# Kernel optimization log

Measured on AMD Instinct MI355X. Metric: run time of the kernel, lower is better.

## Reference

```python
import jax, jax.numpy as jnp
import numpy as np

EPS = 1e-6

def setup_inputs() -> dict:
    key = jax.random.key(0)
    k1, k2, k3 = jax.random.split(key, 3)
    B, N, D = 1, 2048, 1024
    x = jax.random.normal(k1, (B, N, D), dtype=jnp.float32)
    W_qvk = jax.random.normal(k2, (D, 3 * D), dtype=jnp.float32) * (D ** -0.5)
    b_qvk = jax.random.normal(k3, (3 * D,), dtype=jnp.float32) * 0.02
    return {"x": x, "W_qvk": W_qvk, "b_qvk": b_qvk, "head_num": 16}


def _forward(x, W_qvk, b_qvk, head_num):
    B, N, D = x.shape
    qvk = x @ W_qvk + b_qvk                       # (B, N, 3D)
    # torch.chunk order in source: q, v, k
    def to_heads(t):
        return t.reshape(B, N, head_num, D // head_num).transpose(0, 2, 1, 3)  # (B,h,N,e)
    q, v, k = (to_heads(t) for t in jnp.split(qvk, 3, axis=-1))
    e = q.shape[-1]
    # causal linear attention, bucket_size=1
    q = jax.nn.softmax(q, axis=-1) * (e ** -0.5)  # (B,h,N,e)
    k = jnp.exp(k)
    k_cumsum = jnp.cumsum(k, axis=2)              # (B,h,N,e)
    # per-position outer product k_i (x) v_i, then causal prefix-sum over N
    kv = jnp.einsum('bhnd,bhne->bhnde', k, v)     # (B,h,N,e,e)
    kv_cumsum = jnp.cumsum(kv, axis=2)            # (B,h,N,e,e)
    denom = jnp.einsum('bhnd,bhnd->bhn', q, k_cumsum + EPS)   # (B,h,N)
    out = jnp.einsum('bhnd,bhnde->bhne', q, kv_cumsum) / denom[..., None]
    # concat heads: (B,h,N,e) -> (B,N,D)
    return out.transpose(0, 2, 1, 3).reshape(B, N, D)


def reference(x, W_qvk, b_qvk, head_num):
    return _forward(x, W_qvk, b_qvk, head_num)
```

## Files before the change

kernel.cpp:

```cpp
#include <hip/hip_runtime.h>
#include <stdint.h>

#define NTOK 2048
#define NCH 32

typedef __attribute__((ext_vector_type(8))) short bf16x8;
typedef __attribute__((ext_vector_type(8))) unsigned short ushort8v;
typedef __attribute__((ext_vector_type(4))) float f32x4;

__device__ __forceinline__ unsigned short f2bf(float f) {
  unsigned u = __float_as_uint(f);
  u += 0x7fffu + ((u >> 16) & 1u);
  return (unsigned short)(u >> 16);
}
__device__ __forceinline__ float bf2f(unsigned short s) {
  return __uint_as_float(((unsigned)s) << 16);
}

__global__ __launch_bounds__(256) void k_prep_inputs(const float* __restrict__ x,
                                                     unsigned short* __restrict__ xb,
                                                     const float* __restrict__ W,
                                                     unsigned short* __restrict__ Wt) {
  int bid = blockIdx.x;
  if (bid < 2048) {
    int i = (bid * 256 + threadIdx.x) * 4;
    float4 v = *(const float4*)(x + i);
    ushort4 o = { f2bf(v.x), f2bf(v.y), f2bf(v.z), f2bf(v.w) };
    *(ushort4*)(xb + i) = o;
  } else {
    __shared__ float tile[32][33];
    int id = bid - 2048;
    int bx = id % 96, by = id / 96;
    int tx = threadIdx.x & 31, ty = threadIdx.x >> 5;
    int c0 = bx * 32;
    int r0 = by * 32;
#pragma unroll
    for (int j = 0; j < 32; j += 8)
      tile[ty + j][tx] = W[(size_t)(r0 + ty + j) * 3072 + c0 + tx];
    __syncthreads();
#pragma unroll
    for (int j = 0; j < 32; j += 8)
      Wt[(size_t)(c0 + ty + j) * 1024 + r0 + tx] = f2bf(tile[tx][ty + j]);
  }
}

__global__ __launch_bounds__(768, 1) void k_gemm_fused(const unsigned short* __restrict__ xb,
                                                       const unsigned short* __restrict__ wt,
                                                       const float* __restrict__ bias,
                                                       unsigned short* __restrict__ qh,
                                                       unsigned short* __restrict__ kh,
                                                       unsigned short* __restrict__ kt,
                                                       unsigned short* __restrict__ vt) {
  __shared__ __align__(16) unsigned short As[2][128][64];
  __shared__ __align__(16) unsigned short Bs[2][192][64];
  const int t = threadIdx.x;
  const int lane = t & 63;
  const int wave = t >> 6;
  const int wr = wave / 3;
  const int wc = wave % 3;
  const int rowBase = blockIdx.y * 128;
  const int colBase = blockIdx.x * 192;
  const int fr = lane & 15;
  const int khalf = lane >> 4;

  const bool isA = t < 256;
  const int nL = isA ? 4 : 3;
  const int bstr = isA ? 16384 : 24576;
  const unsigned short* gsrc[4];
  char* ldst[4];
#pragma unroll
  for (int j = 0; j < 4; ++j) {
    int idx = isA ? (t + j * 256) : (t - 256 + j * 512);
    if (j >= nL) idx = 0;
    int row = idx >> 3;
    int ssl = (idx & 7) ^ (row & 7);
    gsrc[j] = (isA ? xb + (size_t)(rowBase + row) * 1024
                   : wt + (size_t)(colBase + row) * 1024) + ssl * 8;
    ldst[j] = (isA ? (char*)As : (char*)Bs) + idx * 16;
  }

#define STG(buf, kt0) do {                                                                \
    _Pragma("unroll")                                                                     \
    for (int j_ = 0; j_ < 4; ++j_)                                                        \
      if (j_ < nL)                                                                        \
        __builtin_amdgcn_global_load_lds(                                                 \
            (const __attribute__((address_space(1))) void*)(gsrc[j_] + (kt0) * 64),       \
            (__attribute__((address_space(3))) void*)(ldst[j_] + (buf) * bstr), 16, 0, 0);\
  } while (0)

#define VMW_STEADY() do {                                                                 \
    if (isA) asm volatile("s_waitcnt vmcnt(4)" ::: "memory");                             \
    else     asm volatile("s_waitcnt vmcnt(3)" ::: "memory");                             \
  } while (0)
#define VMCNT0() asm volatile("s_waitcnt vmcnt(0)" ::: "memory")
#define LGKM0()  asm volatile("s_waitcnt lgkmcnt(0)" ::: "memory")
#define BAR()    __builtin_amdgcn_s_barrier()

  f32x4 acc[2][4] = {};
  const int fs0 = khalf ^ (fr & 7);

#define LOAD_FRAGS(cur, af, bff) do {                                                     \
    _Pragma("unroll")                                                                     \
    for (int m = 0; m < 2; ++m) {                                                         \
      const unsigned short* r = &As[cur][wr * 32 + m * 16 + fr][0];                       \
      af[m][0] = *(const bf16x8*)(r + fs0 * 8);                                           \
      af[m][1] = *(const bf16x8*)(r + (fs0 ^ 4) * 8);                                     \
    }                                                                                     \
    _Pragma("unroll")                                                                     \
    for (int n = 0; n < 4; ++n) {                                                         \
      const unsigned short* r = &Bs[cur][wc * 64 + n * 16 + fr][0];                       \
      bff[n][0] = *(const bf16x8*)(r + fs0 * 8);                                          \
      bff[n][1] = *(const bf16x8*)(r + (fs0 ^ 4) * 8);                                    \
    }                                                                                     \
  } while (0)

#define DO_MFMA(af, bff) do {                                                             \
    _Pragma("unroll")                                                                     \
    for (int m = 0; m < 2; ++m)                                                           \
      _Pragma("unroll")                                                                   \
      for (int n = 0; n < 4; ++n) {                                                       \
        acc[m][n] = __builtin_amdgcn_mfma_f32_16x16x32_bf16(af[m][0], bff[n][0], acc[m][n], 0, 0, 0); \
        acc[m][n] = __builtin_amdgcn_mfma_f32_16x16x32_bf16(af[m][1], bff[n][1], acc[m][n], 0, 0, 0); \
      }                                                                                   \
  } while (0)

  STG(0, 0);
  STG(1, 1);
#pragma unroll 1
  for (int ktile = 0; ktile < 14; ++ktile) {
    const int cur = ktile & 1;
    VMW_STEADY();
    BAR();
    bf16x8 af[2][2], bff[4][2];
    LOAD_FRAGS(cur, af, bff);
    LGKM0();
    __builtin_amdgcn_sched_barrier(0);
    BAR();
    STG(cur, ktile + 2);
    __builtin_amdgcn_s_setprio(1);
    DO_MFMA(af, bff);
    __builtin_amdgcn_s_setprio(0);
  }
  {
    VMW_STEADY();
    BAR();
    bf16x8 af[2][2], bff[4][2];
    LOAD_FRAGS(0, af, bff);
    DO_MFMA(af, bff);
  }
  {
    VMCNT0();
    BAR();
    bf16x8 af[2][2], bff[4][2];
    LOAD_FRAGS(1, af, bff);
    DO_MFMA(af, bff);
  }
#undef STG
#undef LOAD_FRAGS
#undef DO_MFMA

  const int g2 = khalf;
  const int ocol = lane & 15;
  const int col0 = colBase + wc * 64;
  const int region = col0 >> 10;
  const int h = (col0 & 1023) >> 6;
  const int r0 = rowBase + wr * 32;
  const int cch = r0 >> 6;
  const int lbase = (wr & 1) * 32;
  float bv[4];
#pragma unroll
  for (int n = 0; n < 4; ++n) bv[n] = bias[col0 + 16 * n + ocol];

  if (region == 0) {
#pragma unroll
    for (int m = 0; m < 2; ++m) {
#pragma unroll
      for (int i = 0; i < 4; ++i) {
        float v[4];
#pragma unroll
        for (int n = 0; n < 4; ++n) v[n] = acc[m][n][i] + bv[n];
        float mx = fmaxf(fmaxf(v[0], v[1]), fmaxf(v[2], v[3]));
#pragma unroll
        for (int off = 1; off <= 8; off <<= 1) mx = fmaxf(mx, __shfl_xor(mx, off));
        float s = 0.f;
#pragma unroll
        for (int n = 0; n < 4; ++n) { v[n] = __expf(v[n] - mx); s += v[n]; }
#pragma unroll
        for (int off = 1; off <= 8; off <<= 1) s += __shfl_xor(s, off);
        float inv = 0.125f / s;
        int tok = r0 + 16 * m + 4 * g2 + i;
        unsigned short* qrow = qh + ((size_t)h * NTOK + tok) * 64;
#pragma unroll
        for (int n = 0; n < 4; ++n) qrow[16 * n + ocol] = f2bf(v[n] * inv);
      }
    }
  } else if (region == 1) {
    unsigned short* vb = vt + (size_t)(h * NCH + cch) * 4096;
#pragma unroll
    for (int m = 0; m < 2; ++m) {
      int tl = lbase + 16 * m + 4 * g2;
#pragma unroll
      for (int n = 0; n < 4; ++n) {
        int e = 16 * n + ocol;
        ushort4 p = { f2bf(acc[m][n][0] + bv[n]), f2bf(acc[m][n][1] + bv[n]),
                      f2bf(acc[m][n][2] + bv[n]), f2bf(acc[m][n][3] + bv[n]) };
        *(ushort4*)&vb[(size_t)e * 64 + tl] = p;
      }
    }
  } else {
    unsigned short* kb = kt + (size_t)(h * NCH + cch) * 4096;
#pragma unroll
    for (int m = 0; m < 2; ++m) {
      int tl = lbase + 16 * m + 4 * g2;
#pragma unroll
      for (int n = 0; n < 4; ++n) {
        int e = 16 * n + ocol;
        float kv[4];
#pragma unroll
        for (int i = 0; i < 4; ++i) kv[i] = __expf(acc[m][n][i] + bv[n]);
        ushort4 p = { f2bf(kv[0]), f2bf(kv[1]), f2bf(kv[2]), f2bf(kv[3]) };
        *(ushort4*)&kb[(size_t)e * 64 + tl] = p;
#pragma unroll
        for (int i = 0; i < 4; ++i)
          kh[((size_t)h * NTOK + r0 + 16 * m + 4 * g2 + i) * 64 + e] = p[i];
      }
    }
  }
}

__global__ __launch_bounds__(256) void k_chunk_sums(const unsigned short* __restrict__ kt,
                                                    const unsigned short* __restrict__ vt,
                                                    float* __restrict__ Sc,
                                                    float* __restrict__ zc) {
  int h = blockIdx.x >> 5, c = blockIdx.x & 31;
  __shared__ __align__(16) unsigned short Kt[64][72], Vt[64][72];
  int t = threadIdx.x, lane = t & 63, w = t >> 6;
  int fr = lane & 15, g = lane >> 4, fko = g * 8;
  const unsigned short* kg = kt + (size_t)(h * NCH + c) * 4096;
  const unsigned short* vg = vt + (size_t)(h * NCH + c) * 4096;
  for (int s = t; s < 512; s += 256) {
    int r = s >> 3, c8 = (s & 7) * 8;
    *(ushort8v*)&Kt[r][c8] = *(const ushort8v*)&kg[r * 64 + c8];
    *(ushort8v*)&Vt[r][c8] = *(const ushort8v*)&vg[r * 64 + c8];
  }
  __syncthreads();
  bf16x8 ka[2];
#pragma unroll
  for (int ks = 0; ks < 2; ++ks) ka[ks] = *(const bf16x8*)&Kt[16 * w + fr][32 * ks + fko];
  f32x4 s4[4] = {};
#pragma unroll
  for (int nb = 0; nb < 4; ++nb)
#pragma unroll
    for (int ks = 0; ks < 2; ++ks) {
      bf16x8 vf = *(const bf16x8*)&Vt[16 * nb + fr][32 * ks + fko];
      s4[nb] = __builtin_amdgcn_mfma_f32_16x16x32_bf16(ka[ks], vf, s4[nb], 0, 0, 0);
    }
  float* so = Sc + (size_t)(h * NCH + c) * 4096;
#pragma unroll
  for (int nb = 0; nb < 4; ++nb) {
    float4 o = { s4[nb][0], s4[nb][1], s4[nb][2], s4[nb][3] };
    *(float4*)&so[(size_t)(16 * nb + fr) * 64 + 16 * w + 4 * g] = o;
  }
  if (w == 0) {
    float z = 0.f;
#pragma unroll
    for (int j = 0; j < 8; ++j) {
      bf16x8 kv = *(const bf16x8*)&Kt[lane][j * 8];
#pragma unroll
      for (int e = 0; e < 8; ++e) z += bf2f((unsigned short)kv[e]);
    }
    zc[(size_t)(h * NCH + c) * 64 + lane] = z;
  }
}

__global__ __launch_bounds__(256) void k_scan(const float* __restrict__ Sc,
                                              unsigned short* __restrict__ Sp,
                                              const float* __restrict__ zc,
                                              float* __restrict__ zp) {
  int b = blockIdx.x;
  if (b < 256) {
    int tg = b * 256 + threadIdx.x;
    int h = tg >> 12, e = tg & 4095;
    float run = 0.f;
    for (int c = 0; c < NCH; ++c) {
      size_t idx = (size_t)(h * NCH + c) * 4096 + e;
      float v = Sc[idx];
      Sp[idx] = f2bf(run);
      run += v;
    }
  } else {
#pragma unroll
    for (int j = 0; j < 4; ++j) {
      int s = threadIdx.x + j * 256;
      int h = s >> 6, d = s & 63;
      float run = 0.f;
      for (int c = 0; c < NCH; ++c) {
        size_t idx = (size_t)(h * NCH + c) * 64 + d;
        zp[idx] = run;
        run += zc[idx];
      }
    }
  }
}

__global__ __launch_bounds__(256) void k_attn(const unsigned short* __restrict__ qh,
                                              const unsigned short* __restrict__ kh,
                                              const unsigned short* __restrict__ vt,
                                              const unsigned short* __restrict__ Sp,
                                              const float* __restrict__ zp,
                                              float* __restrict__ out) {
  int h = blockIdx.x >> 5, c = blockIdx.x & 31;
  __shared__ __align__(16) unsigned short Qs[64][72], Ks[64][72], Vts[64][72], Sts[64][72], Ams[64][72];
  __shared__ float zs[64], denom[64];
  int t = threadIdx.x, lane = t & 63, w = t >> 6;
  int fr = lane & 15, g = lane >> 4, fko = g * 8;
  const unsigned short* qg = qh + ((size_t)h * NTOK + c * 64) * 64;
  const unsigned short* kg = kh + ((size_t)h * NTOK + c * 64) * 64;
  const unsigned short* vg = vt + (size_t)(h * NCH + c) * 4096;
  const unsigned short* sg = Sp + (size_t)(h * NCH + c) * 4096;
  for (int s = t; s < 512; s += 256) {
    int r = s >> 3, c8 = (s & 7) * 8;
    *(ushort8v*)&Qs[r][c8]  = *(const ushort8v*)&qg[r * 64 + c8];
    *(ushort8v*)&Ks[r][c8]  = *(const ushort8v*)&kg[r * 64 + c8];
    *(ushort8v*)&Vts[r][c8] = *(const ushort8v*)&vg[r * 64 + c8];
    *(ushort8v*)&Sts[r][c8] = *(const ushort8v*)&sg[r * 64 + c8];
  }
  if (t < 64) zs[t] = zp[(size_t)(h * NCH + c) * 64 + t];
  __syncthreads();

  bf16x8 qa[2];
#pragma unroll
  for (int ks = 0; ks < 2; ++ks) qa[ks] = *(const bf16x8*)&Qs[16 * w + fr][32 * ks + fko];
  f32x4 a1[4] = {};
#pragma unroll
  for (int mb = 0; mb < 4; ++mb)
#pragma unroll
    for (int ks = 0; ks < 2; ++ks) {
      bf16x8 kf = *(const bf16x8*)&Ks[16 * mb + fr][32 * ks + fko];
      a1[mb] = __builtin_amdgcn_mfma_f32_16x16x32_bf16(qa[ks], kf, a1[mb], 0, 0, 0);
    }
#pragma unroll
  for (int i = 0; i < 4; ++i) {
    int n = 16 * w + 4 * g + i;
    float rs = 0.f;
#pragma unroll
    for (int j = 0; j < 4; ++j) rs += bf2f(Qs[n][fr * 4 + j]) * zs[fr * 4 + j];
#pragma unroll
    for (int mb = 0; mb < 4; ++mb) {
      int m = 16 * mb + fr;
      float v = (m <= n) ? a1[mb][i] : 0.f;
      a1[mb][i] = v;
      rs += v;
      Ams[n][16 * mb + fr] = f2bf(v);
    }
#pragma unroll
    for (int off = 1; off <= 8; off <<= 1) rs += __shfl_xor(rs, off);
    if (fr == 0) denom[n] = rs + 1.25e-7f;
  }
  __syncthreads();

  bf16x8 xa[4];
#pragma unroll
  for (int ks = 0; ks < 2; ++ks) {
    xa[ks]     = *(const bf16x8*)&Vts[16 * w + fr][32 * ks + fko];
    xa[2 + ks] = *(const bf16x8*)&Sts[16 * w + fr][32 * ks + fko];
  }
  f32x4 o4[4] = {};
#pragma unroll
  for (int nb = 0; nb < 4; ++nb)
#pragma unroll
    for (int ks = 0; ks < 2; ++ks) {
      bf16x8 afr = *(const bf16x8*)&Ams[16 * nb + fr][32 * ks + fko];
      o4[nb] = __builtin_amdgcn_mfma_f32_16x16x32_bf16(xa[ks], afr, o4[nb], 0, 0, 0);
      bf16x8 qfr = *(const bf16x8*)&Qs[16 * nb + fr][32 * ks + fko];
      o4[nb] = __builtin_amdgcn_mfma_f32_16x16x32_bf16(xa[2 + ks], qfr, o4[nb], 0, 0, 0);
    }
#pragma unroll
  for (int nb = 0; nb < 4; ++nb) {
    int n = 16 * nb + fr;
    float dv = denom[n];
    float4 res = { o4[nb][0] / dv, o4[nb][1] / dv, o4[nb][2] / dv, o4[nb][3] / dv };
    *(float4*)&out[(size_t)(c * 64 + n) * 1024 + h * 64 + 16 * w + 4 * g] = res;
  }
}

extern "C" void kernel_launch(void* const* d_in, const int* in_sizes, int n_in,
                              void* d_out, int out_size, void* d_ws, size_t ws_size,
                              hipStream_t stream) {
  (void)in_sizes; (void)n_in; (void)out_size; (void)ws_size;
  const float* x = (const float*)d_in[0];
  const float* W = (const float*)d_in[1];
  const float* b = (const float*)d_in[2];
  char* ws = (char*)d_ws;

  const size_t MB = 1024 * 1024;
  unsigned short* xb = (unsigned short*)(ws + 0);
  unsigned short* Wt = (unsigned short*)(ws + 4 * MB);
  unsigned short* qh = (unsigned short*)(ws + 10 * MB);
  unsigned short* kh = (unsigned short*)(ws + 14 * MB);
  unsigned short* kt = (unsigned short*)(ws + 18 * MB);
  unsigned short* vt = (unsigned short*)(ws + 22 * MB);
  float*          Sc = (float*)(ws + 26 * MB);
  unsigned short* Sp = (unsigned short*)(ws + 34 * MB);
  float*          zc = (float*)(ws + 38 * MB);
  float*          zp = (float*)(ws + 38 * MB + 131072);

  k_prep_inputs<<<dim3(5120), dim3(256), 0, stream>>>(x, xb, W, Wt);
  k_gemm_fused<<<dim3(16, 16), dim3(768), 0, stream>>>(xb, Wt, b, qh, kh, kt, vt);
  k_chunk_sums<<<dim3(512), dim3(256), 0, stream>>>(kt, vt, Sc, zc);
  k_scan<<<dim3(257), dim3(256), 0, stream>>>(Sc, Sp, zc, zp);
  k_attn<<<dim3(512), dim3(256), 0, stream>>>(qh, kh, vt, Sp, zp, (float*)d_out);
}
```

Baseline: 48.41 us.

## Fuse chunk sums and scan into one MFMA-accumulating kernel, move key sums into GEMM

Replaces the separate chunk-sum and scan kernels with a single kernel in which each block walks the chunks sequentially, accumulates the K^T V state in MFMA registers and writes the exclusive prefix directly as bf16. This removes the fp32 Sc round trip through memory and one launch. Per-chunk key sums are now computed in the GEMM epilogue with shuffles and atomics into a zeroed buffer, and the attention kernel forms the prefix of those sums itself. The cost is a 64-block serial scan over 32 chunks with low parallelism, plus an added memset and atomics.

```diff
diff --git a/kernel.cpp b/kernel.cpp
--- a/kernel.cpp
+++ b/kernel.cpp
@@ -50,7 +50,8 @@
                                                        unsigned short* __restrict__ qh,
                                                        unsigned short* __restrict__ kh,
                                                        unsigned short* __restrict__ kt,
-                                                       unsigned short* __restrict__ vt) {
+                                                       unsigned short* __restrict__ vt,
+                                                       float* __restrict__ zc) {
   __shared__ __align__(16) unsigned short As[2][128][64];
   __shared__ __align__(16) unsigned short Bs[2][192][64];
   const int t = threadIdx.x;
@@ -209,6 +210,7 @@
     }
   } else {
     unsigned short* kb = kt + (size_t)(h * NCH + cch) * 4096;
+    float pz[4] = {0.f, 0.f, 0.f, 0.f};
 #pragma unroll
     for (int m = 0; m < 2; ++m) {
       int tl = lbase + 16 * m + 4 * g2;
@@ -218,6 +220,7 @@
         float kv[4];
 #pragma unroll
         for (int i = 0; i < 4; ++i) kv[i] = __expf(acc[m][n][i] + bv[n]);
+        pz[n] += kv[0] + kv[1] + kv[2] + kv[3];
         ushort4 p = { f2bf(kv[0]), f2bf(kv[1]), f2bf(kv[2]), f2bf(kv[3]) };
         *(ushort4*)&kb[(size_t)e * 64 + tl] = p;
 #pragma unroll
@@ -225,81 +228,39 @@
           kh[((size_t)h * NTOK + r0 + 16 * m + 4 * g2 + i) * 64 + e] = p[i];
       }
     }
-  }
-}
-
-__global__ __launch_bounds__(256) void k_chunk_sums(const unsigned short* __restrict__ kt,
-                                                    const unsigned short* __restrict__ vt,
-                                                    float* __restrict__ Sc,
-                                                    float* __restrict__ zc) {
-  int h = blockIdx.x >> 5, c = blockIdx.x & 31;
-  __shared__ __align__(16) unsigned short Kt[64][72], Vt[64][72];
-  int t = threadIdx.x, lane = t & 63, w = t >> 6;
-  int fr = lane & 15, g = lane >> 4, fko = g * 8;
-  const unsigned short* kg = kt + (size_t)(h * NCH + c) * 4096;
-  const unsigned short* vg = vt + (size_t)(h * NCH + c) * 4096;
-  for (int s = t; s < 512; s += 256) {
-    int r = s >> 3, c8 = (s & 7) * 8;
-    *(ushort8v*)&Kt[r][c8] = *(const ushort8v*)&kg[r * 64 + c8];
-    *(ushort8v*)&Vt[r][c8] = *(const ushort8v*)&vg[r * 64 + c8];
-  }
-  __syncthreads();
-  bf16x8 ka[2];
-#pragma unroll
-  for (int ks = 0; ks < 2; ++ks) ka[ks] = *(const bf16x8*)&Kt[16 * w + fr][32 * ks + fko];
-  f32x4 s4[4] = {};
-#pragma unroll
-  for (int nb = 0; nb < 4; ++nb)
-#pragma unroll
-    for (int ks = 0; ks < 2; ++ks) {
-      bf16x8 vf = *(const bf16x8*)&Vt[16 * nb + fr][32 * ks + fko];
-      s4[nb] = __builtin_amdgcn_mfma_f32_16x16x32_bf16(ka[ks], vf, s4[nb], 0, 0, 0);
-    }
-  float* so = Sc + (size_t)(h * NCH + c) * 4096;
-#pragma unroll
-  for (int nb = 0; nb < 4; ++nb) {
-    float4 o = { s4[nb][0], s4[nb][1], s4[nb][2], s4[nb][3] };
-    *(float4*)&so[(size_t)(16 * nb + fr) * 64 + 16 * w + 4 * g] = o;
-  }
-  if (w == 0) {
-    float z = 0.f;
-#pragma unroll
-    for (int j = 0; j < 8; ++j) {
-      bf16x8 kv = *(const bf16x8*)&Kt[lane][j * 8];
-#pragma unroll
-      for (int e = 0; e < 8; ++e) z += bf2f((unsigned short)kv[e]);
-    }
-    zc[(size_t)(h * NCH + c) * 64 + lane] = z;
-  }
-}
-
-__global__ __launch_bounds__(256) void k_scan(const float* __restrict__ Sc,
-                                              unsigned short* __restrict__ Sp,
-                                              const float* __restrict__ zc,
-                                              float* __restrict__ zp) {
-  int b = blockIdx.x;
-  if (b < 256) {
-    int tg = b * 256 + threadIdx.x;
-    int h = tg >> 12, e = tg & 4095;
-    float run = 0.f;
-    for (int c = 0; c < NCH; ++c) {
-      size_t idx = (size_t)(h * NCH + c) * 4096 + e;
-      float v = Sc[idx];
-      Sp[idx] = f2bf(run);
-      run += v;
-    }
-  } else {
-#pragma unroll
-    for (int j = 0; j < 4; ++j) {
-      int s = threadIdx.x + j * 256;
-      int h = s >> 6, d = s & 63;
-      float run = 0.f;
-      for (int c = 0; c < NCH; ++c) {
-        size_t idx = (size_t)(h * NCH + c) * 64 + d;
-        zp[idx] = run;
-        run += zc[idx];
-      }
-    }
+#pragma unroll
+    for (int n = 0; n < 4; ++n) {
+      pz[n] += __shfl_xor(pz[n], 16);
+      pz[n] += __shfl_xor(pz[n], 32);
+    }
+    if (g2 == 0) {
+      float* zrow = zc + (size_t)(h * NCH + cch) * 64;
+#pragma unroll
+      for (int n = 0; n < 4; ++n) atomicAdd(&zrow[16 * n + ocol], pz[n]);
+    }
+  }
+}
+
+__global__ __launch_bounds__(256) void k_sumscan(const unsigned short* __restrict__ kt,
+                                                 const unsigned short* __restrict__ vt,
+                                                 unsigned short* __restrict__ Sp) {
+  const int h = blockIdx.x >> 2, q = blockIdx.x & 3;
+  const int t = threadIdx.x, lane = t & 63, w = t >> 6;
+  const int fr = lane & 15, g = lane >> 4, fko = g * 8;
+  const unsigned short* kbase = kt + (size_t)h * NCH * 4096 + (16 * w + fr) * 64 + fko;
+  const unsigned short* vbase = vt + (size_t)h * NCH * 4096 + (q * 16 + fr) * 64 + fko;
+  unsigned short* spb = Sp + (size_t)h * NCH * 4096 + (q * 16 + fr) * 64 + 16 * w + 4 * g;
+  f32x4 run = {};
+#pragma unroll 2
+  for (int c = 0; c < NCH; ++c) {
+    bf16x8 ka0 = *(const bf16x8*)(kbase + (size_t)c * 4096);
+    bf16x8 ka1 = *(const bf16x8*)(kbase + (size_t)c * 4096 + 32);
+    bf16x8 vf0 = *(const bf16x8*)(vbase + (size_t)c * 4096);
+    bf16x8 vf1 = *(const bf16x8*)(vbase + (size_t)c * 4096 + 32);
+    ushort4 o = { f2bf(run[0]), f2bf(run[1]), f2bf(run[2]), f2bf(run[3]) };
+    *(ushort4*)(spb + (size_t)c * 4096) = o;
+    run = __builtin_amdgcn_mfma_f32_16x16x32_bf16(ka0, vf0, run, 0, 0, 0);
+    run = __builtin_amdgcn_mfma_f32_16x16x32_bf16(ka1, vf1, run, 0, 0, 0);
   }
 }
 
@@ -307,7 +268,7 @@
                                               const unsigned short* __restrict__ kh,
                                               const unsigned short* __restrict__ vt,
                                               const unsigned short* __restrict__ Sp,
-                                              const float* __restrict__ zp,
+                                              const float* __restrict__ zc,
                                               float* __restrict__ out) {
   int h = blockIdx.x >> 5, c = blockIdx.x & 31;
   __shared__ __align__(16) unsigned short Qs[64][72], Ks[64][72], Vts[64][72], Sts[64][72], Ams[64][72];
@@ -325,7 +286,19 @@
     *(ushort8v*)&Vts[r][c8] = *(const ushort8v*)&vg[r * 64 + c8];
     *(ushort8v*)&Sts[r][c8] = *(const ushort8v*)&sg[r * 64 + c8];
   }
-  if (t < 64) zs[t] = zp[(size_t)(h * NCH + c) * 64 + t];
+  if (t < 64) {
+    const float* zb = zc + (size_t)h * NCH * 64 + t;
+    float z0 = 0.f, z1 = 0.f, z2 = 0.f, z3 = 0.f;
+    int cc = 0;
+    for (; cc + 4 <= c; cc += 4) {
+      z0 += zb[(size_t)cc * 64];
+      z1 += zb[(size_t)(cc + 1) * 64];
+      z2 += zb[(size_t)(cc + 2) * 64];
+      z3 += zb[(size_t)(cc + 3) * 64];
+    }
+    for (; cc < c; ++cc) z0 += zb[(size_t)cc * 64];
+    zs[t] = (z0 + z1) + (z2 + z3);
+  }
   __syncthreads();
 
   bf16x8 qa[2];
@@ -400,14 +373,12 @@
   unsigned short* kh = (unsigned short*)(ws + 14 * MB);
   unsigned short* kt = (unsigned short*)(ws + 18 * MB);
   unsigned short* vt = (unsigned short*)(ws + 22 * MB);
-  float*          Sc = (float*)(ws + 26 * MB);
-  unsigned short* Sp = (unsigned short*)(ws + 34 * MB);
-  float*          zc = (float*)(ws + 38 * MB);
-  float*          zp = (float*)(ws + 38 * MB + 131072);
-
+  unsigned short* Sp = (unsigned short*)(ws + 26 * MB);
+  float*          zc = (float*)(ws + 30 * MB);
+
+  hipMemsetAsync(zc, 0, (size_t)16 * 32 * 64 * sizeof(float), stream);
   k_prep_inputs<<<dim3(5120), dim3(256), 0, stream>>>(x, xb, W, Wt);
-  k_gemm_fused<<<dim3(16, 16), dim3(768), 0, stream>>>(xb, Wt, b, qh, kh, kt, vt);
-  k_chunk_sums<<<dim3(512), dim3(256), 0, stream>>>(kt, vt, Sc, zc);
-  k_scan<<<dim3(257), dim3(256), 0, stream>>>(Sc, Sp, zc, zp);
-  k_attn<<<dim3(512), dim3(256), 0, stream>>>(qh, kh, vt, Sp, zp, (float*)d_out);
-}
+  k_gemm_fused<<<dim3(16, 16), dim3(768), 0, stream>>>(xb, Wt, b, qh, kh, kt, vt, zc);
+  k_sumscan<<<dim3(64), dim3(256), 0, stream>>>(kt, vt, Sp);
+  k_attn<<<dim3(512), dim3(256), 0, stream>>>(qh, kh, vt, Sp, zc, (float*)d_out);
+}
```

New measurement: 63.48 us. 1.31x slower.
